# Optimization experiments

Hardware: AMD Instinct MI355X
Metric: run time of the kernel (lower is better)

The kernel has to match this reference:

```python
import jax, jax.numpy as jnp
import numpy as np

DIM = 1024
NE = 4            # num_experts
MLP = 4           # mlp_ratio
H = 16            # num_heads
HD = DIM // H     # head dim
EXP = 3 * DIM + MLP * DIM   # expand output dim (7*dim)
CIN = DIM + MLP * DIM       # contract input dim (5*dim)


def layer_norm(x, g, b, eps=1e-5):
    m = jnp.mean(x, axis=-1, keepdims=True)
    v = jnp.var(x, axis=-1, keepdims=True)
    return (x - m) * jax.lax.rsqrt(v + eps) * g + b


def setup_inputs() -> dict:
    key = jax.random.key(0)
    ks = jax.random.split(key, 8)
    B, N = 8, 1024
    x = jax.random.normal(ks[0], (B, N, DIM), jnp.float32)
    expert_mask = jax.random.randint(ks[1], (B, N), 0, NE, jnp.int32)
    router_probs = jax.random.uniform(ks[2], (B, N, NE), jnp.float32)
    expand_weight = jax.random.normal(ks[3], (EXP, DIM), jnp.float32) * 0.02
    mlp_bias = jnp.zeros((MLP * DIM,), jnp.float32)
    contract_weight = jax.random.normal(ks[4], (2 * DIM, CIN), jnp.float32) * 0.02
    contract_bias = jnp.zeros((2 * DIM,), jnp.float32)
    norm1_g = jnp.ones((DIM,), jnp.float32)
    norm1_b = jnp.zeros((DIM,), jnp.float32)
    norm2_g = jnp.ones((DIM,), jnp.float32)
    norm2_b = jnp.zeros((DIM,), jnp.float32)
    alpha = jnp.zeros((1,), jnp.float32)
    return dict(x=x, expert_mask=expert_mask, router_probs=router_probs,
                expand_weight=expand_weight, mlp_bias=mlp_bias,
                contract_weight=contract_weight, contract_bias=contract_bias,
                norm1_g=norm1_g, norm1_b=norm1_b, norm2_g=norm2_g, norm2_b=norm2_b,
                alpha=alpha)


def reference(x, expert_mask, router_probs, expand_weight, mlp_bias,
              contract_weight, contract_bias, norm1_g, norm1_b,
              norm2_g, norm2_b, alpha):
    B, N, _ = x.shape
    shift = (NE - 1 - expert_mask).astype(jnp.int32)          # [B,N]
    # nested (matryoshka) active dims per token
    d_in = DIM // jnp.left_shift(1, shift)                    # expand: active input dims
    d_out = (2 * DIM) // jnp.left_shift(1, shift)             # contract: active output dims

    # nested_linear_expand: zero inactive input features, then full GEMM
    in_mask = (jnp.arange(DIM) < d_in[..., None]).astype(x.dtype)
    xn = layer_norm(x, norm1_g, norm1_b) * in_mask
    y = jnp.einsum('bnd,od->bno', xn, expand_weight)          # [B,N,7*dim]

    qkv = y[..., :3 * DIM]
    mlp_hidden = y[..., 3 * DIM:] + mlp_bias

    q = qkv[..., :DIM]
    k = layer_norm(qkv[..., DIM:2 * DIM], norm2_g, norm2_b)
    v = layer_norm(qkv[..., 2 * DIM:], norm2_g, norm2_b)

    qh = q.reshape(B, N, H, HD)
    kh = k.reshape(B, N, H, HD)
    vh = v.reshape(B, N, H, HD)
    scale = HD ** -0.5
    attn = jax.nn.softmax(jnp.einsum('bqhd,bkhd->bhqk', qh, kh) * scale, axis=-1)
    attn_out = jnp.einsum('bhqk,bkhd->bqhd', attn, vh).reshape(B, N, DIM)

    h = jnp.concatenate([attn_out, jax.nn.gelu(mlp_hidden, approximate=False)], axis=-1)
    # nested_linear_contract: full GEMM, zero inactive output features
    z = jnp.einsum('bnc,oc->bno', h, contract_weight) + contract_bias  # [B,N,2*dim]
    z = z * (jnp.arange(2 * DIM) < d_out[..., None]).astype(z.dtype)

    attn_o = z[..., :DIM] + x
    mlp_o = z[..., DIM:]
    expert_probs = jnp.take_along_axis(router_probs, expert_mask[..., None].astype(jnp.int32), axis=-1)  # [B,N,1]
    out = attn_o + (alpha * expert_probs + 1.0) * mlp_o
    return (out, expert_mask, router_probs)
```

## Files before the change

kernel.cpp:

```cpp
#include <hip/hip_runtime.h>
#include <hip/hip_bf16.h>
#include <math.h>

typedef __bf16 bf16_t;
typedef __attribute__((ext_vector_type(8))) __bf16 bf16x8;
typedef __attribute__((ext_vector_type(4))) __bf16 bf16x4;
typedef __attribute__((ext_vector_type(4))) float f32x4;
typedef __attribute__((ext_vector_type(4))) unsigned u32x4;

typedef __attribute__((address_space(1))) unsigned as1u;
typedef __attribute__((address_space(3))) unsigned as3u;

#define MAXT1 68
#define MAXJ2 2112

__device__ __forceinline__ void async_copy16(bf16_t* lds, const bf16_t* g) {
  __builtin_amdgcn_global_load_lds((as1u*)g, (as3u*)lds, 16, 0, 0);
}

__device__ __forceinline__ float gelu_exact(float t) {
  return 0.5f * t * (1.0f + erff(t * 0.70710678118654752f));
}

__device__ __forceinline__ unsigned pack_bf16(float a, float b) {
  unsigned short ha = __builtin_bit_cast(unsigned short, (bf16_t)a);
  unsigned short hb = __builtin_bit_cast(unsigned short, (bf16_t)b);
  return (unsigned)ha | ((unsigned)hb << 16);
}

__global__ __launch_bounds__(256)
void cast_kernel(const float* __restrict__ w, bf16_t* __restrict__ o, int n) {
  int i = (blockIdx.x * 256 + threadIdx.x) * 4;
  if (i < n) {
    float4 v = *(const float4*)(w + i);
    bf16x4 t;
    t[0] = (bf16_t)v.x; t[1] = (bf16_t)v.y; t[2] = (bf16_t)v.z; t[3] = (bf16_t)v.w;
    *(bf16x4*)(o + i) = t;
  }
}

__global__ __launch_bounds__(1024)
void sort_kernel(const int* __restrict__ em, int* __restrict__ perm,
                 int* __restrict__ t1, int* __restrict__ j2) {
  __shared__ int cnt[4], cur[4], tb[5], jb[5];
  const int tid = threadIdx.x;
  const int wave = tid >> 6, lane = tid & 63;
  if (tid < 4) cnt[tid] = 0;
  __syncthreads();
  for (int c = wave; c < 128; c += 16) {
    int e = em[c * 64 + lane];
    unsigned long long m0 = __ballot(e == 0), m1 = __ballot(e == 1);
    unsigned long long m2 = __ballot(e == 2), m3 = __ballot(e == 3);
    if (lane == 0) {
      atomicAdd(&cnt[0], (int)__popcll(m0)); atomicAdd(&cnt[1], (int)__popcll(m1));
      atomicAdd(&cnt[2], (int)__popcll(m2)); atomicAdd(&cnt[3], (int)__popcll(m3));
    }
  }
  __syncthreads();
  if (tid == 0) {
    cur[0] = 0; cur[1] = cnt[0]; cur[2] = cnt[0] + cnt[1]; cur[3] = cnt[0] + cnt[1] + cnt[2];
    tb[0] = 0; jb[0] = 0;
    for (int i = 0; i < 4; ++i) {
      int e = 3 - i;
      int nt = (cnt[e] + 127) >> 7;
      tb[i + 1] = tb[i] + nt;
      jb[i + 1] = jb[i] + nt * (4 << e);
    }
  }
  __syncthreads();
  for (int c = wave; c < 128; c += 16) {
    int i = c * 64 + lane;
    int e = em[i];
    unsigned long long m0 = __ballot(e == 0), m1 = __ballot(e == 1);
    unsigned long long m2 = __ballot(e == 2), m3 = __ballot(e == 3);
    unsigned long long me = e == 0 ? m0 : e == 1 ? m1 : e == 2 ? m2 : m3;
    int bl = 0;
    if (lane < 4) {
      unsigned long long ml = lane == 0 ? m0 : lane == 1 ? m1 : lane == 2 ? m2 : m3;
      bl = atomicAdd(&cur[lane], (int)__popcll(ml));
    }
    int base = __shfl(bl, e);
    unsigned long long lt = (1ull << lane) - 1ull;
    perm[base + (int)__popcll(me & lt)] = i;
  }
  int offp[5];
  offp[0] = 0;
  #pragma unroll
  for (int e = 0; e < 4; ++e) offp[e + 1] = offp[e] + cnt[e];
  for (int t = tid; t < MAXT1; t += 1024) {
    int e = -1, loc = 0;
    #pragma unroll
    for (int i = 0; i < 4; ++i) if (t >= tb[i] && t < tb[i + 1]) { e = 3 - i; loc = t - tb[i]; }
    if (e >= 0) {
      t1[t * 3] = e; t1[t * 3 + 1] = offp[e] + loc * 128;
      t1[t * 3 + 2] = min(128, cnt[e] - loc * 128);
    } else t1[t * 3] = -1;
  }
  for (int j = tid; j < MAXJ2; j += 1024) {
    int e = -1, loc = 0;
    #pragma unroll
    for (int i = 0; i < 4; ++i) if (j >= jb[i] && j < jb[i + 1]) { e = 3 - i; loc = j - jb[i]; }
    if (e >= 0) {
      int t = loc >> (2 + e), b = loc & ((4 << e) - 1);
      j2[j * 4] = e; j2[j * 4 + 1] = offp[e] + t * 128;
      j2[j * 4 + 2] = min(128, cnt[e] - t * 128); j2[j * 4 + 3] = b;
    } else j2[j * 4] = -1;
  }
}

__global__ __launch_bounds__(256)
void ln1_kernel(const float* __restrict__ x, const float* __restrict__ gam,
                const float* __restrict__ bet, const int* __restrict__ em,
                bf16_t* __restrict__ xn) {
  const int row = blockIdx.x, tid = threadIdx.x;
  const float4 v = ((const float4*)(x + (size_t)row * 1024))[tid];
  float s = v.x + v.y + v.z + v.w;
  float sq = v.x * v.x + v.y * v.y + v.z * v.z + v.w * v.w;
  #pragma unroll
  for (int off = 1; off < 64; off <<= 1) { s += __shfl_xor(s, off); sq += __shfl_xor(sq, off); }
  __shared__ float red[8];
  const int wave = tid >> 6, lane = tid & 63;
  if (lane == 0) { red[wave] = s; red[4 + wave] = sq; }
  __syncthreads();
  s = red[0] + red[1] + red[2] + red[3];
  sq = red[4] + red[5] + red[6] + red[7];
  const float mean = s * (1.0f / 1024.0f);
  const float var = sq * (1.0f / 1024.0f) - mean * mean;
  const float rstd = rsqrtf(var + 1e-5f);
  const int din = 1024 >> (3 - em[row]);
  const float4 gv = ((const float4*)gam)[tid];
  const float4 bv = ((const float4*)bet)[tid];
  const int c0 = tid * 4;
  float vf[4] = {v.x, v.y, v.z, v.w};
  float gf[4] = {gv.x, gv.y, gv.z, gv.w};
  float bvf[4] = {bv.x, bv.y, bv.z, bv.w};
  bf16x4 o;
  #pragma unroll
  for (int i = 0; i < 4; ++i) {
    float t = (vf[i] - mean) * rstd * gf[i] + bvf[i];
    o[i] = (c0 + i < din) ? (bf16_t)t : (bf16_t)0.0f;
  }
  *(bf16x4*)(xn + (size_t)row * 1024 + c0) = o;
}

__global__ __launch_bounds__(256)
void ln2_kernel(bf16_t* __restrict__ kv, const float* __restrict__ gam,
                const float* __restrict__ bet) {
  const int row = blockIdx.x, tid = threadIdx.x;
  bf16_t* base = kv + (size_t)row * 2048;
  bf16x4 kk = *(const bf16x4*)(base + tid * 4);
  bf16x4 vv = *(const bf16x4*)(base + 1024 + tid * 4);
  float kf[4], vf[4];
  float ks = 0, ksq = 0, vs = 0, vsq = 0;
  #pragma unroll
  for (int i = 0; i < 4; ++i) {
    kf[i] = (float)kk[i]; ks += kf[i]; ksq += kf[i] * kf[i];
    vf[i] = (float)vv[i]; vs += vf[i]; vsq += vf[i] * vf[i];
  }
  #pragma unroll
  for (int off = 1; off < 64; off <<= 1) {
    ks += __shfl_xor(ks, off); ksq += __shfl_xor(ksq, off);
    vs += __shfl_xor(vs, off); vsq += __shfl_xor(vsq, off);
  }
  __shared__ float red[16];
  const int wave = tid >> 6, lane = tid & 63;
  if (lane == 0) { red[wave] = ks; red[4 + wave] = ksq; red[8 + wave] = vs; red[12 + wave] = vsq; }
  __syncthreads();
  ks = red[0] + red[1] + red[2] + red[3];
  ksq = red[4] + red[5] + red[6] + red[7];
  vs = red[8] + red[9] + red[10] + red[11];
  vsq = red[12] + red[13] + red[14] + red[15];
  const float mk = ks * (1.f / 1024.f), mv = vs * (1.f / 1024.f);
  const float rk = rsqrtf(ksq * (1.f / 1024.f) - mk * mk + 1e-5f);
  const float rv = rsqrtf(vsq * (1.f / 1024.f) - mv * mv + 1e-5f);
  const float4 gv = ((const float4*)gam)[tid];
  const float4 bv = ((const float4*)bet)[tid];
  float gf[4] = {gv.x, gv.y, gv.z, gv.w}, bvf[4] = {bv.x, bv.y, bv.z, bv.w};
  bf16x4 ko, vo;
  #pragma unroll
  for (int i = 0; i < 4; ++i) {
    ko[i] = (bf16_t)((kf[i] - mk) * rk * gf[i] + bvf[i]);
    vo[i] = (bf16_t)((vf[i] - mv) * rv * gf[i] + bvf[i]);
  }
  *(bf16x4*)(base + tid * 4) = ko;
  *(bf16x4*)(base + 1024 + tid * 4) = vo;
}

__global__ __launch_bounds__(256)
void vt_kernel(const bf16_t* __restrict__ kv, bf16_t* __restrict__ vT) {
  __shared__ bf16_t t[64][80];
  const int tt = blockIdx.x, head = blockIdx.y;
  const int tid = threadIdx.x;
  const int r8 = tid >> 3, c8 = tid & 7;
  #pragma unroll
  for (int i = 0; i < 2; ++i) {
    const int tok = i * 32 + r8;
    bf16x8 v = *(const bf16x8*)(kv + (size_t)(tt * 64 + tok) * 2048 + 1024 + head * 64 + c8 * 8);
    #pragma unroll
    for (int j = 0; j < 8; ++j) t[c8 * 8 + j][tok] = v[j];
  }
  __syncthreads();
  const int bb = tt >> 4;
  const int tloc = (tt & 15) * 64;
  #pragma unroll
  for (int i = 0; i < 2; ++i) {
    const int d = i * 32 + r8;
    bf16x8 v = *(const bf16x8*)(&t[d][c8 * 8]);
    *(bf16x8*)(vT + (size_t)((bb * 16 + head) * 64 + d) * 1024 + tloc + c8 * 8) = v;
  }
}

#define STAGE(BUF, KT) do { \
    bf16_t* As_ = SMEM + (BUF) * BUFE; \
    bf16_t* Bs_ = As_ + 8192; \
    _Pragma("unroll") \
    for (int i_ = 0; i_ < 4; ++i_) \
      async_copy16(As_ + (i_ * 256 + wave * 64) * 8, Ag[i_] + (KT) * 64); \
    _Pragma("unroll") \
    for (int i_ = 0; i_ < NI; ++i_) \
      async_copy16(Bs_ + (i_ * 256 + wave * 64) * 8, Wg + (size_t)(i_ * 32) * K + (size_t)(KT) * 64); \
  } while (0)

template<int EPI>
__global__ __launch_bounds__(256)
void gemm_bt(const bf16_t* __restrict__ A, const bf16_t* __restrict__ W,
             const int* __restrict__ perm, const int* __restrict__ desc,
             const float* __restrict__ bias,
             bf16_t* __restrict__ hb, bf16_t* __restrict__ kvb,
             bf16_t* __restrict__ z) {
  constexpr int K = (EPI == 0) ? 1024 : 5120;
  constexpr int BN = (EPI == 0) ? 128 : 64;
  constexpr int NI = BN / 32;
  constexpr int WC = BN / 2;
  constexpr int BUFE = 8192 + BN * 64;
  const int* d = desc + ((EPI == 0) ? blockIdx.y * 3 : blockIdx.x * 4);
  const int e = d[0];
  if (e < 0) return;
  const int nval = d[2];
  const int bn = (EPI == 0) ? blockIdx.x : d[3];
  const int nkt = (EPI == 0) ? (2 << e) : 80;

  __shared__ bf16_t SMEM[2 * BUFE];
  __shared__ int prow[128];
  const int tid = threadIdx.x;
  if (tid < 128) prow[tid] = perm[d[1] + min(tid, nval - 1)];
  const int wave = tid >> 6, lane = tid & 63;
  const int l15 = lane & 15, l4 = lane >> 4;
  const int wm = wave >> 1, wn = wave & 1;

  f32x4 acc[4][NI] = {};

  const int rbase = tid >> 3;
  const int ss = (tid & 7) ^ (rbase & 7);
  __syncthreads();
  const bf16_t* Ag[4];
  #pragma unroll
  for (int i = 0; i < 4; ++i) Ag[i] = A + (size_t)prow[i * 32 + rbase] * K + ss * 8;
  const bf16_t* Wg = W + (size_t)(bn * BN + rbase) * K + ss * 8;

  STAGE(0, 0);
  __syncthreads();

  for (int kt = 0; kt < nkt; ++kt) {
    if (kt + 1 < nkt) STAGE((kt + 1) & 1, kt + 1);
    const bf16_t* Asr = SMEM + (kt & 1) * BUFE;
    const bf16_t* Bsr = Asr + 8192;
    #pragma unroll
    for (int ks = 0; ks < 2; ++ks) {
      bf16x8 a[4], b[NI];
      #pragma unroll
      for (int mi = 0; mi < 4; ++mi) {
        const int r = wm * 64 + mi * 16 + l15;
        const int slot = (ks * 4 + l4) ^ (r & 7);
        a[mi] = *(const bf16x8*)(Asr + r * 64 + slot * 8);
      }
      #pragma unroll
      for (int ni = 0; ni < NI; ++ni) {
        const int r = wn * WC + ni * 16 + l15;
        const int slot = (ks * 4 + l4) ^ (r & 7);
        b[ni] = *(const bf16x8*)(Bsr + r * 64 + slot * 8);
      }
      #pragma unroll
      for (int mi = 0; mi < 4; ++mi)
        #pragma unroll
        for (int ni = 0; ni < NI; ++ni)
          acc[mi][ni] = __builtin_amdgcn_mfma_f32_16x16x32_bf16(a[mi], b[ni], acc[mi][ni], 0, 0, 0);
    }
    __syncthreads();
  }

  #pragma unroll
  for (int mi = 0; mi < 4; ++mi) {
    #pragma unroll
    for (int ni = 0; ni < NI; ++ni) {
      const int colf = wn * WC + ni * 16 + l15;
      #pragma unroll
      for (int r = 0; r < 4; ++r) {
        const int row = wm * 64 + mi * 16 + l4 * 4 + r;
        const float c = acc[mi][ni][r];
        bf16_t v;
        if (EPI == 0) {
          const int gc = bn * 128 + colf;
          v = (gc >= 3072) ? (bf16_t)gelu_exact(c + bias[gc - 3072]) : (bf16_t)c;
        } else {
          v = (bf16_t)(c + bias[bn * 64 + colf]);
        }
        SMEM[row * 136 + colf] = v;
      }
    }
  }
  __syncthreads();
  if (EPI == 0) {
    const int col0 = (tid & 15) * 8;
    const int gc0 = bn * 128 + col0;
    #pragma unroll
    for (int i = 0; i < 8; ++i) {
      const int row = (tid >> 4) * 8 + i;
      if (row < nval) {
        const size_t token = (size_t)prow[row];
        bf16x8 v = *(const bf16x8*)(SMEM + row * 136 + col0);
        if (gc0 < 1024)      *(bf16x8*)(hb + token * 5120 + gc0) = v;
        else if (gc0 < 3072) *(bf16x8*)(kvb + token * 2048 + (gc0 - 1024)) = v;
        else                 *(bf16x8*)(hb + token * 5120 + 1024 + (gc0 - 3072)) = v;
      }
    }
  } else {
    const int col0 = (tid & 7) * 8;
    const int gc0 = bn * 64 + col0;
    #pragma unroll
    for (int i = 0; i < 4; ++i) {
      const int row = (tid >> 3) * 4 + i;
      if (row < nval) {
        const size_t token = (size_t)prow[row];
        bf16x8 v = *(const bf16x8*)(SMEM + row * 136 + col0);
        *(bf16x8*)(z + token * 2048 + gc0) = v;
      }
    }
  }
}

__global__ __launch_bounds__(256)
void attn_kernel(const bf16_t* __restrict__ kv, const bf16_t* __restrict__ vT,
                 bf16_t* __restrict__ hb) {
  __shared__ bf16_t Kl[64 * 64];
  __shared__ bf16_t Vl[64 * 64];
  const int tid = threadIdx.x;
  const int wave = tid >> 6, lane = tid & 63;
  const int l15 = lane & 15, l4 = lane >> 4;
  const int qt = blockIdx.x, bh = blockIdx.y;
  const int bb = bh >> 4;
  const int tok0 = bb << 10;
  const int d0 = (bh & 15) << 6;

  const int qrow = tok0 + qt * 64 + wave * 16 + l15;
  const bf16x8 bq0 = *(const bf16x8*)(hb + (size_t)qrow * 5120 + d0 + l4 * 8);
  const bf16x8 bq1 = *(const bf16x8*)(hb + (size_t)qrow * 5120 + d0 + 32 + l4 * 8);

  f32x4 o[4] = {};
  float mrun = -1e30f, lrun = 0.f;

  const int krb = tid >> 3;
  const int kss = (tid & 7) ^ (krb & 7);
  const int idx0 = ((2 * (l4 & 1) + 0) * 16 + l15) * 4;
  const int idx1 = ((2 * (l4 & 1) + 1) * 16 + l15) * 4;
  const bool hi = (l4 >> 1) != 0;

  for (int kt = 0; kt < 16; ++kt) {
    const int krow0 = tok0 + kt * 64;
    #pragma unroll
    for (int i = 0; i < 2; ++i) {
      async_copy16(Kl + (i * 256 + wave * 64) * 8,
                   kv + (size_t)(krow0 + i * 32 + krb) * 2048 + d0 + kss * 8);
      async_copy16(Vl + (i * 256 + wave * 64) * 8,
                   vT + (size_t)(bh * 64 + i * 32 + krb) * 1024 + kt * 64 + kss * 8);
    }
    __syncthreads();

    f32x4 s[4] = {};
    __builtin_amdgcn_s_setprio(1);
    #pragma unroll
    for (int ks = 0; ks < 2; ++ks) {
      const bf16x8 bq = ks ? bq1 : bq0;
      #pragma unroll
      for (int kc = 0; kc < 4; ++kc) {
        const int r = kc * 16 + l15;
        const int slot = (ks * 4 + l4) ^ (r & 7);
        bf16x8 ak = *(const bf16x8*)(Kl + r * 64 + slot * 8);
        s[kc] = __builtin_amdgcn_mfma_f32_16x16x32_bf16(ak, bq, s[kc], 0, 0, 0);
      }
    }
    __builtin_amdgcn_s_setprio(0);

    float mx = s[0][0];
    #pragma unroll
    for (int kc = 0; kc < 4; ++kc)
      #pragma unroll
      for (int r = 0; r < 4; ++r) mx = fmaxf(mx, s[kc][r]);
    mx = fmaxf(mx, __shfl_xor(mx, 16));
    mx = fmaxf(mx, __shfl_xor(mx, 32));
    mx *= 0.125f;
    const float mnew = fmaxf(mrun, mx);
    const float corr = __expf(mrun - mnew);
    float ps = 0.f;
    #pragma unroll
    for (int kc = 0; kc < 4; ++kc)
      #pragma unroll
      for (int r = 0; r < 4; ++r) {
        const float p = __expf(s[kc][r] * 0.125f - mnew);
        s[kc][r] = p;
        ps += p;
      }
    ps += __shfl_xor(ps, 16);
    ps += __shfl_xor(ps, 32);
    lrun = lrun * corr + ps;
    mrun = mnew;

    unsigned pd[4][2], bp[4][2][2];
    #pragma unroll
    for (int kc = 0; kc < 4; ++kc) {
      pd[kc][0] = pack_bf16(s[kc][0], s[kc][1]);
      pd[kc][1] = pack_bf16(s[kc][2], s[kc][3]);
    }
    #pragma unroll
    for (int kc = 0; kc < 4; ++kc)
      #pragma unroll
      for (int rp = 0; rp < 2; ++rp) {
        bp[kc][rp][0] = (unsigned)__builtin_amdgcn_ds_bpermute(idx0, (int)pd[kc][rp]);
        bp[kc][rp][1] = (unsigned)__builtin_amdgcn_ds_bpermute(idx1, (int)pd[kc][rp]);
      }
    u32x4 w0, w1;
    w0[0] = hi ? bp[1][0][0] : bp[0][0][0];
    w0[1] = hi ? bp[1][1][0] : bp[0][1][0];
    w0[2] = hi ? bp[1][0][1] : bp[0][0][1];
    w0[3] = hi ? bp[1][1][1] : bp[0][1][1];
    w1[0] = hi ? bp[3][0][0] : bp[2][0][0];
    w1[1] = hi ? bp[3][1][0] : bp[2][1][0];
    w1[2] = hi ? bp[3][0][1] : bp[2][0][1];
    w1[3] = hi ? bp[3][1][1] : bp[2][1][1];
    const bf16x8 pa0 = __builtin_bit_cast(bf16x8, w0);
    const bf16x8 pa1 = __builtin_bit_cast(bf16x8, w1);

    float cq[4];
    #pragma unroll
    for (int r = 0; r < 4; ++r) cq[r] = __shfl(corr, l4 * 4 + r);
    #pragma unroll
    for (int dn = 0; dn < 4; ++dn)
      #pragma unroll
      for (int r = 0; r < 4; ++r) o[dn][r] *= cq[r];

    __builtin_amdgcn_s_setprio(1);
    #pragma unroll
    for (int dn = 0; dn < 4; ++dn) {
      const int r = dn * 16 + l15;
      bf16x8 bv0 = *(const bf16x8*)(Vl + r * 64 + ((l4 ^ (r & 7)) * 8));
      bf16x8 bv1 = *(const bf16x8*)(Vl + r * 64 + (((4 + l4) ^ (r & 7)) * 8));
      o[dn] = __builtin_amdgcn_mfma_f32_16x16x32_bf16(pa0, bv0, o[dn], 0, 0, 0);
      o[dn] = __builtin_amdgcn_mfma_f32_16x16x32_bf16(pa1, bv1, o[dn], 0, 0, 0);
    }
    __builtin_amdgcn_s_setprio(0);
    __syncthreads();
  }

  const float il = 1.0f / lrun;
  float linv[4];
  #pragma unroll
  for (int r = 0; r < 4; ++r) linv[r] = __shfl(il, l4 * 4 + r);
  #pragma unroll
  for (int r = 0; r < 4; ++r) {
    const int gq = tok0 + qt * 64 + wave * 16 + l4 * 4 + r;
    #pragma unroll
    for (int dn = 0; dn < 4; ++dn)
      hb[(size_t)gq * 5120 + d0 + dn * 16 + l15] = (bf16_t)(o[dn][r] * linv[r]);
  }
}

__global__ __launch_bounds__(256)
void final_kernel(const bf16_t* __restrict__ z, const float* __restrict__ x,
                  const int* __restrict__ em, const float* __restrict__ rp,
                  const float* __restrict__ alpha, float* __restrict__ out) {
  const int row = blockIdx.x, tid = threadIdx.x;
  const int e = em[row];
  const int dout = 2048 >> (3 - e);
  const float f = alpha[0] * rp[row * 4 + e] + 1.0f;
  const bf16x4 z0 = ((const bf16x4*)(z + (size_t)row * 2048))[tid];
  const bf16x4 z1 = ((const bf16x4*)(z + (size_t)row * 2048 + 1024))[tid];
  const float4 xv = ((const float4*)(x + (size_t)row * 1024))[tid];
  const int c = tid * 4;
  float4 o;
  o.x = ((c + 0) < dout ? (float)z0[0] : 0.f) + xv.x + f * ((1024 + c + 0) < dout ? (float)z1[0] : 0.f);
  o.y = ((c + 1) < dout ? (float)z0[1] : 0.f) + xv.y + f * ((1024 + c + 1) < dout ? (float)z1[1] : 0.f);
  o.z = ((c + 2) < dout ? (float)z0[2] : 0.f) + xv.z + f * ((1024 + c + 2) < dout ? (float)z1[2] : 0.f);
  o.w = ((c + 3) < dout ? (float)z0[3] : 0.f) + xv.w + f * ((1024 + c + 3) < dout ? (float)z1[3] : 0.f);
  ((float4*)(out + (size_t)row * 1024))[tid] = o;
  float* out_em = out + 8388608;
  float* out_rp = out_em + 8192;
  if (tid == 0) out_em[row] = (float)e;
  if (tid < 4) out_rp[row * 4 + tid] = rp[row * 4 + tid];
}

extern "C" void kernel_launch(void* const* d_in, const int* in_sizes, int n_in,
                              void* d_out, int out_size, void* d_ws, size_t ws_size,
                              hipStream_t stream) {
  const float* x = (const float*)d_in[0];
  const int* em = (const int*)d_in[1];
  const float* rp = (const float*)d_in[2];
  const float* w_exp = (const float*)d_in[3];
  const float* mlp_bias = (const float*)d_in[4];
  const float* w_con = (const float*)d_in[5];
  const float* c_bias = (const float*)d_in[6];
  const float* n1g = (const float*)d_in[7];
  const float* n1b = (const float*)d_in[8];
  const float* n2g = (const float*)d_in[9];
  const float* n2b = (const float*)d_in[10];
  const float* alpha = (const float*)d_in[11];

  char* ws = (char*)d_ws;
  bf16_t* Wexp = (bf16_t*)ws;
  bf16_t* xn   = (bf16_t*)(ws + 14680064);
  bf16_t* vT   = (bf16_t*)(ws + 14680064);
  int*    perm = (int*)(ws + 31457280);
  int*    t1d  = (int*)(ws + 31457280 + 32768);
  int*    j2d  = (int*)(ws + 31457280 + 34816);
  bf16_t* kvb  = (bf16_t*)(ws + 48234496);
  bf16_t* z    = (bf16_t*)(ws + 48234496);
  bf16_t* Wcon = (bf16_t*)(ws + 81788928);
  bf16_t* hb   = (bf16_t*)(ws + 102760448);

  sort_kernel<<<1, 1024, 0, stream>>>(em, perm, t1d, j2d);
  cast_kernel<<<7168, 256, 0, stream>>>(w_exp, Wexp, 7340032);
  cast_kernel<<<10240, 256, 0, stream>>>(w_con, Wcon, 10485760);
  ln1_kernel<<<8192, 256, 0, stream>>>(x, n1g, n1b, em, xn);
  gemm_bt<0><<<dim3(56, MAXT1), 256, 0, stream>>>(xn, Wexp, perm, t1d, mlp_bias,
                                                  hb, kvb, nullptr);
  ln2_kernel<<<8192, 256, 0, stream>>>(kvb, n2g, n2b);
  vt_kernel<<<dim3(128, 16), 256, 0, stream>>>(kvb, vT);
  attn_kernel<<<dim3(16, 128), 256, 0, stream>>>(kvb, vT, hb);
  gemm_bt<1><<<MAXJ2, 256, 0, stream>>>(hb, Wcon, perm, j2d, c_bias,
                                        nullptr, nullptr, z);
  final_kernel<<<8192, 256, 0, stream>>>(z, x, em, rp, alpha, (float*)d_out);
}
```

Baseline: 439.3 us.

## Remap GEMM block indices so row tiles spread evenly across XCDs

Both grouped GEMMs now map blocks to work with the MI355X's chiplets in mind. Blocks are dispatched round-robin across 8 XCDs, so block p lands on XCD p&7. The expand GEMM becomes a 1D grid in which each row tile's 56 column blocks all land on the same XCD. The contract GEMM's job list is interleaved per XCD, assigning tiles to XCDs in turn. The aim is better L2 reuse of the A rows within each XCD and balanced load across XCDs, at the cost of a larger sparse job table (MAXJ2 grows, with more early-exit blocks) and extra serial setup in the sort kernel.

New measurement: 466.8 us. 1.06x slower.

```diff
diff --git a/kernel.cpp b/kernel.cpp
--- a/kernel.cpp
+++ b/kernel.cpp
@@ -12,7 +12,8 @@
 typedef __attribute__((address_space(3))) unsigned as3u;
 
 #define MAXT1 68
-#define MAXJ2 2112
+#define MAXJ2 2560
+#define G1GRID 4032
 
 __device__ __forceinline__ void async_copy16(bf16_t* lds, const bf16_t* g) {
   __builtin_amdgcn_global_load_lds((as1u*)g, (as3u*)lds, 16, 0, 0);
@@ -42,7 +43,9 @@
 __global__ __launch_bounds__(1024)
 void sort_kernel(const int* __restrict__ em, int* __restrict__ perm,
                  int* __restrict__ t1, int* __restrict__ j2) {
-  __shared__ int cnt[4], cur[4], tb[5], jb[5];
+  __shared__ int cnt[4], cur[4];
+  __shared__ int te[MAXT1], trow[MAXT1], tnv[MAXT1], txcd[MAXT1], tjb[MAXT1];
+  __shared__ int ntiles;
   const int tid = threadIdx.x;
   const int wave = tid >> 6, lane = tid & 63;
   if (tid < 4) cnt[tid] = 0;
@@ -59,13 +62,24 @@
   __syncthreads();
   if (tid == 0) {
     cur[0] = 0; cur[1] = cnt[0]; cur[2] = cnt[0] + cnt[1]; cur[3] = cnt[0] + cnt[1] + cnt[2];
-    tb[0] = 0; jb[0] = 0;
+    int offp[5];
+    offp[0] = 0;
+    for (int e = 0; e < 4; ++e) offp[e + 1] = offp[e] + cnt[e];
+    int xjobs[8] = {0, 0, 0, 0, 0, 0, 0, 0};
+    int T = 0;
     for (int i = 0; i < 4; ++i) {
       int e = 3 - i;
       int nt = (cnt[e] + 127) >> 7;
-      tb[i + 1] = tb[i] + nt;
-      jb[i + 1] = jb[i] + nt * (4 << e);
-    }
+      for (int loc = 0; loc < nt; ++loc) {
+        te[T] = e; trow[T] = offp[e] + loc * 128;
+        tnv[T] = min(128, cnt[e] - loc * 128);
+        int x = T & 7;
+        txcd[T] = x; tjb[T] = xjobs[x];
+        xjobs[x] += (4 << e);
+        ++T;
+      }
+    }
+    ntiles = T;
   }
   __syncthreads();
   for (int c = wave; c < 128; c += 16) {
@@ -83,28 +97,22 @@
     unsigned long long lt = (1ull << lane) - 1ull;
     perm[base + (int)__popcll(me & lt)] = i;
   }
-  int offp[5];
-  offp[0] = 0;
-  #pragma unroll
-  for (int e = 0; e < 4; ++e) offp[e + 1] = offp[e] + cnt[e];
   for (int t = tid; t < MAXT1; t += 1024) {
-    int e = -1, loc = 0;
-    #pragma unroll
-    for (int i = 0; i < 4; ++i) if (t >= tb[i] && t < tb[i + 1]) { e = 3 - i; loc = t - tb[i]; }
-    if (e >= 0) {
-      t1[t * 3] = e; t1[t * 3 + 1] = offp[e] + loc * 128;
-      t1[t * 3 + 2] = min(128, cnt[e] - loc * 128);
-    } else t1[t * 3] = -1;
-  }
-  for (int j = tid; j < MAXJ2; j += 1024) {
-    int e = -1, loc = 0;
-    #pragma unroll
-    for (int i = 0; i < 4; ++i) if (j >= jb[i] && j < jb[i + 1]) { e = 3 - i; loc = j - jb[i]; }
-    if (e >= 0) {
-      int t = loc >> (2 + e), b = loc & ((4 << e) - 1);
-      j2[j * 4] = e; j2[j * 4 + 1] = offp[e] + t * 128;
-      j2[j * 4 + 2] = min(128, cnt[e] - t * 128); j2[j * 4 + 3] = b;
-    } else j2[j * 4] = -1;
+    if (t < ntiles) { t1[t * 3] = te[t]; t1[t * 3 + 1] = trow[t]; t1[t * 3 + 2] = tnv[t]; }
+    else t1[t * 3] = -1;
+  }
+  for (int j = tid; j < MAXJ2; j += 1024) j2[j * 4] = -1;
+  __syncthreads();
+  for (int base = 0; base < MAXT1 * 32; base += 1024) {
+    int idx = base + tid;
+    int T = idx >> 5, b = idx & 31;
+    if (T < ntiles && b < (4 << te[T])) {
+      int p = txcd[T] + 8 * (tjb[T] + b);
+      if (p < MAXJ2) {
+        j2[p * 4] = te[T]; j2[p * 4 + 1] = trow[T];
+        j2[p * 4 + 2] = tnv[T]; j2[p * 4 + 3] = b;
+      }
+    }
   }
 }
 
@@ -233,17 +241,30 @@
   constexpr int NI = BN / 32;
   constexpr int WC = BN / 2;
   constexpr int BUFE = 8192 + BN * 64;
-  const int* d = desc + ((EPI == 0) ? blockIdx.y * 3 : blockIdx.x * 4);
-  const int e = d[0];
-  if (e < 0) return;
-  const int nval = d[2];
-  const int bn = (EPI == 0) ? blockIdx.x : d[3];
-  const int nkt = (EPI == 0) ? (2 << e) : 80;
+
+  int e, d1, nval, bn, nkt;
+  if (EPI == 0) {
+    const int p = blockIdx.x;
+    const int x = p & 7, k = p >> 3;
+    const int tloc = k / 56;
+    bn = k % 56;
+    const int t = tloc * 8 + x;
+    if (t >= MAXT1) return;
+    const int* d = desc + t * 3;
+    e = d[0];
+    if (e < 0) return;
+    d1 = d[1]; nval = d[2]; nkt = 2 << e;
+  } else {
+    const int* d = desc + blockIdx.x * 4;
+    e = d[0];
+    if (e < 0) return;
+    d1 = d[1]; nval = d[2]; bn = d[3]; nkt = 80;
+  }
 
   __shared__ bf16_t SMEM[2 * BUFE];
   __shared__ int prow[128];
   const int tid = threadIdx.x;
-  if (tid < 128) prow[tid] = perm[d[1] + min(tid, nval - 1)];
+  if (tid < 128) prow[tid] = perm[d1 + min(tid, nval - 1)];
   const int wave = tid >> 6, lane = tid & 63;
   const int l15 = lane & 15, l4 = lane >> 4;
   const int wm = wave >> 1, wn = wave & 1;
@@ -530,8 +551,8 @@
   cast_kernel<<<7168, 256, 0, stream>>>(w_exp, Wexp, 7340032);
   cast_kernel<<<10240, 256, 0, stream>>>(w_con, Wcon, 10485760);
   ln1_kernel<<<8192, 256, 0, stream>>>(x, n1g, n1b, em, xn);
-  gemm_bt<0><<<dim3(56, MAXT1), 256, 0, stream>>>(xn, Wexp, perm, t1d, mlp_bias,
-                                                  hb, kvb, nullptr);
+  gemm_bt<0><<<G1GRID, 256, 0, stream>>>(xn, Wexp, perm, t1d, mlp_bias,
+                                         hb, kvb, nullptr);
   ln2_kernel<<<8192, 256, 0, stream>>>(kvb, n2g, n2b);
   vt_kernel<<<dim3(128, 16), 256, 0, stream>>>(kvb, vT);
   attn_kernel<<<dim3(16, 128), 256, 0, stream>>>(kvb, vT, hb);
```
